# Kernel optimization log

Hardware: AMD Instinct MI355X
Metric: run time of the kernel (lower is better)

Reference implementation:

```python
import jax, jax.numpy as jnp
import numpy as np


def setup_inputs() -> dict:
    key = jax.random.key(0)
    # x: [B, C, T, M] = [64, 4, 8192, 16]
    x = jax.random.normal(key, (64, 4, 8192, 16), dtype=jnp.float32)
    return {"x": x}


def reference(x) -> jnp.ndarray:
    # torch.cov(row[c].T): variables = last dim M, observations = T, correction=1.
    # Output: [B, C, M, M]
    T = x.shape[2]
    xc = x - jnp.mean(x, axis=2, keepdims=True)        # center over time axis
    cov = jnp.einsum('bctm,bctn->bcmn', xc, xc) / (T - 1)
    return cov
```

## Files before the change

### kernel.cpp

```cpp
#include <hip/hip_runtime.h>


constexpr int T_DIM = 8192;
constexpr int M_DIM = 16;
constexpr int NPAIR = 136;
constexpr int BLOCK = 512;
constexpr int NACC  = M_DIM + NPAIR;

__global__ __launch_bounds__(BLOCK, 2)
void cov_kernel(const float* __restrict__ x, float* __restrict__ out) {
    const int bc  = blockIdx.x;
    const int tid = threadIdx.x;
    const float* __restrict__ xin = x + (size_t)bc * (size_t)(T_DIM * M_DIM);

    float s[M_DIM];
    float p[NPAIR];
#pragma unroll
    for (int i = 0; i < M_DIM; ++i) s[i] = 0.0f;
#pragma unroll
    for (int i = 0; i < NPAIR; ++i) p[i] = 0.0f;

#pragma unroll 2
    for (int it = 0; it < T_DIM / BLOCK; ++it) {
        const int r = tid + it * BLOCK;
        const float4* __restrict__ rp = (const float4*)(xin + r * M_DIM);
        const float4 v0 = rp[0];
        const float4 v1 = rp[1];
        const float4 v2 = rp[2];
        const float4 v3 = rp[3];
        const float row[M_DIM] = {v0.x, v0.y, v0.z, v0.w,
                                  v1.x, v1.y, v1.z, v1.w,
                                  v2.x, v2.y, v2.z, v2.w,
                                  v3.x, v3.y, v3.z, v3.w};
#pragma unroll
        for (int m = 0; m < M_DIM; ++m) s[m] += row[m];
        int idx = 0;
#pragma unroll
        for (int m = 0; m < M_DIM; ++m) {
#pragma unroll
            for (int n = m; n < M_DIM; ++n) {
                p[idx++] += row[m] * row[n];
            }
        }
    }

#pragma unroll
    for (int off = 32; off > 0; off >>= 1) {
#pragma unroll
        for (int i = 0; i < M_DIM; ++i) s[i] += __shfl_down(s[i], off, 64);
#pragma unroll
        for (int i = 0; i < NPAIR; ++i) p[i] += __shfl_down(p[i], off, 64);
    }

    __shared__ float red[BLOCK / 64][NACC];
    __shared__ float tot[NACC];
    const int wave = tid >> 6;
    const int lane = tid & 63;
    if (lane == 0) {
#pragma unroll
        for (int i = 0; i < M_DIM; ++i) red[wave][i] = s[i];
#pragma unroll
        for (int i = 0; i < NPAIR; ++i) red[wave][M_DIM + i] = p[i];
    }
    __syncthreads();
    if (tid < NACC) {
        float a = 0.0f;
#pragma unroll
        for (int w = 0; w < BLOCK / 64; ++w) a += red[w][tid];
        tot[tid] = a;
    }
    __syncthreads();

    if (tid < M_DIM * M_DIM) {
        const int m = tid >> 4;
        const int n = tid & 15;
        const int mm = m < n ? m : n;
        const int nn = m < n ? n : m;
        const int idx = mm * M_DIM - (mm * (mm + 1)) / 2 + nn;
        const float Sm = tot[m];
        const float Sn = tot[n];
        const float P  = tot[M_DIM + idx];
        const float cov = (P - Sm * Sn * (1.0f / (float)T_DIM))
                        * (1.0f / (float)(T_DIM - 1));
        out[(size_t)bc * (M_DIM * M_DIM) + tid] = cov;
    }
}

extern "C" void kernel_launch(void* const* d_in, const int* in_sizes, int n_in,
                              void* d_out, int out_size, void* d_ws, size_t ws_size,
                              hipStream_t stream) {
    const float* x = (const float*)d_in[0];
    float* out = (float*)d_out;
    const int n_bc = in_sizes[0] / (T_DIM * M_DIM);
    cov_kernel<<<dim3(n_bc), dim3(BLOCK), 0, stream>>>(x, out);
}
```

Measured before the change: 216.5 us.

## Compute covariance Gram matrix with bf16 MFMA instead of per-thread FMAs

Replaces the per-thread 136-pair fp32 outer-product accumulation with a per-wave 16x16x32 bf16 MFMA. Each lane loads eight time rows of one feature column and rounds them to bf16 to form the fragment, so the Gram matrix comes out directly in MFMA accumulator layout. Blocks grow to 1024 threads, each wave owns a contiguous time slice, and the per-feature sums stay fp32. This removes the heavy register pressure and the long shuffle reduction of 152 accumulators. In exchange, the products lose precision through bf16 rounding inside an uncentered covariance formula, and the global loads become strided scalar reads.

```diff
diff --git a/kernel.cpp b/kernel.cpp
--- a/kernel.cpp
+++ b/kernel.cpp
@@ -3,86 +3,82 @@
 
 constexpr int T_DIM = 8192;
 constexpr int M_DIM = 16;
-constexpr int NPAIR = 136;
-constexpr int BLOCK = 512;
-constexpr int NACC  = M_DIM + NPAIR;
+constexpr int BLOCK = 1024;
+constexpr int NWAVE = BLOCK / 64;
+constexpr int T_PER_WAVE = T_DIM / NWAVE;
+constexpr int CHUNKS = T_PER_WAVE / 32;
 
-__global__ __launch_bounds__(BLOCK, 2)
+using bf16x8 = __attribute__((ext_vector_type(8))) short;
+using f32x4  = __attribute__((ext_vector_type(4))) float;
+
+static __device__ inline short f2bf(float f) {
+    union { float f; unsigned u; } v{f};
+    unsigned r = v.u + 0x7fffu + ((v.u >> 16) & 1u);
+    return (short)(r >> 16);
+}
+
+__global__ __launch_bounds__(BLOCK)
 void cov_kernel(const float* __restrict__ x, float* __restrict__ out) {
-    const int bc  = blockIdx.x;
-    const int tid = threadIdx.x;
-    const float* __restrict__ xin = x + (size_t)bc * (size_t)(T_DIM * M_DIM);
+    const int bc   = blockIdx.x;
+    const int tid  = threadIdx.x;
+    const int wave = tid >> 6;
+    const int lane = tid & 63;
+    const int q    = lane >> 4;
+    const int m    = lane & 15;
 
-    float s[M_DIM];
-    float p[NPAIR];
-#pragma unroll
-    for (int i = 0; i < M_DIM; ++i) s[i] = 0.0f;
-#pragma unroll
-    for (int i = 0; i < NPAIR; ++i) p[i] = 0.0f;
+    const int t0 = wave * T_PER_WAVE + q * 8;
+    const float* __restrict__ base =
+        x + (size_t)bc * (T_DIM * M_DIM) + (size_t)t0 * M_DIM + m;
+
+    f32x4 acc = {0.f, 0.f, 0.f, 0.f};
+    float sum = 0.f;
 
 #pragma unroll 2
-    for (int it = 0; it < T_DIM / BLOCK; ++it) {
-        const int r = tid + it * BLOCK;
-        const float4* __restrict__ rp = (const float4*)(xin + r * M_DIM);
-        const float4 v0 = rp[0];
-        const float4 v1 = rp[1];
-        const float4 v2 = rp[2];
-        const float4 v3 = rp[3];
-        const float row[M_DIM] = {v0.x, v0.y, v0.z, v0.w,
-                                  v1.x, v1.y, v1.z, v1.w,
-                                  v2.x, v2.y, v2.z, v2.w,
-                                  v3.x, v3.y, v3.z, v3.w};
-#pragma unroll
-        for (int m = 0; m < M_DIM; ++m) s[m] += row[m];
-        int idx = 0;
-#pragma unroll
-        for (int m = 0; m < M_DIM; ++m) {
-#pragma unroll
-            for (int n = m; n < M_DIM; ++n) {
-                p[idx++] += row[m] * row[n];
-            }
-        }
+    for (int c = 0; c < CHUNKS; ++c) {
+        const float* __restrict__ p = base + (size_t)c * 32 * M_DIM;
+        float f0 = p[0 * M_DIM], f1 = p[1 * M_DIM];
+        float f2 = p[2 * M_DIM], f3 = p[3 * M_DIM];
+        float f4 = p[4 * M_DIM], f5 = p[5 * M_DIM];
+        float f6 = p[6 * M_DIM], f7 = p[7 * M_DIM];
+        sum += ((f0 + f1) + (f2 + f3)) + ((f4 + f5) + (f6 + f7));
+        bf16x8 frag;
+        frag[0] = f2bf(f0); frag[1] = f2bf(f1);
+        frag[2] = f2bf(f2); frag[3] = f2bf(f3);
+        frag[4] = f2bf(f4); frag[5] = f2bf(f5);
+        frag[6] = f2bf(f6); frag[7] = f2bf(f7);
+        acc = __builtin_amdgcn_mfma_f32_16x16x32_bf16(frag, frag, acc, 0, 0, 0);
     }
 
+    sum += __shfl_xor(sum, 16, 64);
+    sum += __shfl_xor(sum, 32, 64);
+
+    __shared__ float Pred[NWAVE][256];
+    __shared__ float Sred[NWAVE][M_DIM];
+    __shared__ float Stot[M_DIM];
+
 #pragma unroll
-    for (int off = 32; off > 0; off >>= 1) {
+    for (int r = 0; r < 4; ++r)
+        Pred[wave][(q * 4 + r) * M_DIM + m] = acc[r];
+    if (lane < M_DIM) Sred[wave][lane] = sum;
+    __syncthreads();
+
+    if (tid < M_DIM) {
+        float s = 0.f;
 #pragma unroll
-        for (int i = 0; i < M_DIM; ++i) s[i] += __shfl_down(s[i], off, 64);
-#pragma unroll
-        for (int i = 0; i < NPAIR; ++i) p[i] += __shfl_down(p[i], off, 64);
-    }
-
-    __shared__ float red[BLOCK / 64][NACC];
-    __shared__ float tot[NACC];
-    const int wave = tid >> 6;
-    const int lane = tid & 63;
-    if (lane == 0) {
-#pragma unroll
-        for (int i = 0; i < M_DIM; ++i) red[wave][i] = s[i];
-#pragma unroll
-        for (int i = 0; i < NPAIR; ++i) red[wave][M_DIM + i] = p[i];
-    }
-    __syncthreads();
-    if (tid < NACC) {
-        float a = 0.0f;
-#pragma unroll
-        for (int w = 0; w < BLOCK / 64; ++w) a += red[w][tid];
-        tot[tid] = a;
+        for (int w = 0; w < NWAVE; ++w) s += Sred[w][tid];
+        Stot[tid] = s;
     }
     __syncthreads();
 
-    if (tid < M_DIM * M_DIM) {
-        const int m = tid >> 4;
-        const int n = tid & 15;
-        const int mm = m < n ? m : n;
-        const int nn = m < n ? n : m;
-        const int idx = mm * M_DIM - (mm * (mm + 1)) / 2 + nn;
-        const float Sm = tot[m];
-        const float Sn = tot[n];
-        const float P  = tot[M_DIM + idx];
-        const float cov = (P - Sm * Sn * (1.0f / (float)T_DIM))
+    if (tid < 256) {
+        float P = 0.f;
+#pragma unroll
+        for (int w = 0; w < NWAVE; ++w) P += Pred[w][tid];
+        const int mi = tid >> 4;
+        const int ni = tid & 15;
+        const float cov = (P - Stot[mi] * Stot[ni] * (1.0f / (float)T_DIM))
                         * (1.0f / (float)(T_DIM - 1));
-        out[(size_t)bc * (M_DIM * M_DIM) + tid] = cov;
+        out[(size_t)bc * 256 + tid] = cov;
     }
 }
 
```

New measurement: 187.6 us. -13.3%, faster.
